# Performance work log

Measured on AMD Instinct MI355X. Metric: run time of the kernel, lower is better.

The kernel has to match this reference:

```python
import jax, jax.numpy as jnp
import numpy as np

N_NODES = 100000
N_EDGES = 1600000
NEG_SLOPE = 0.2  # DGL GATConv default leaky_relu slope
BN_EPS = 1e-5


def setup_inputs() -> dict:
    key = jax.random.key(0)
    ks = jax.random.split(key, 10)
    feats = jax.random.normal(ks[0], (N_NODES, 128), dtype=jnp.float32)
    src = jax.random.randint(ks[1], (N_EDGES,), 0, N_NODES, dtype=jnp.int64)
    dst = jax.random.randint(ks[2], (N_EDGES,), 0, N_NODES, dtype=jnp.int64)
    fc_w = jax.random.normal(ks[3], (256, 128), dtype=jnp.float32) * 0.05   # H*D x in_feats
    attn_l = jax.random.normal(ks[4], (4, 64), dtype=jnp.float32) * 0.05
    attn_r = jax.random.normal(ks[5], (4, 64), dtype=jnp.float32) * 0.05
    res_w = jax.random.normal(ks[6], (256, 128), dtype=jnp.float32) * 0.05  # residual projection
    bias = jax.random.normal(ks[7], (4, 64), dtype=jnp.float32) * 0.05
    gamma = jnp.ones((64,), dtype=jnp.float32)
    beta = jnp.zeros((64,), dtype=jnp.float32)
    return {"feats": feats, "src": src, "dst": dst, "fc_w": fc_w,
            "attn_l": attn_l, "attn_r": attn_r, "res_w": res_w,
            "bias": bias, "gamma": gamma, "beta": beta}


def reference(feats, src, dst, fc_w, attn_l, attn_r, res_w, bias, gamma, beta):
    N = feats.shape[0]
    H, D = attn_l.shape
    # projected features [N, H, D] (feat_drop is identity in eval mode)
    h = (feats @ fc_w.T).reshape(N, H, D)
    # per-node attention logits [N, H]
    el = jnp.sum(h * attn_l[None], axis=-1)
    er = jnp.sum(h * attn_r[None], axis=-1)
    # edge logits, leaky relu
    e = el[src] + er[dst]                       # [E, H]
    e = jnp.where(e > 0, e, NEG_SLOPE * e)
    # numerically stable segment softmax over incoming edges of each dst node
    m = jax.ops.segment_max(e, dst, num_segments=N)       # [N, H]
    ex = jnp.exp(e - m[dst])                               # [E, H]
    s = jax.ops.segment_sum(ex, dst, num_segments=N)       # [N, H]
    alpha = ex / s[dst]                                    # [E, H]
    # weighted message aggregation: scatter-add alpha * h_src into dst
    msg = h[src] * alpha[:, :, None]                       # [E, H, D]
    rst = jax.ops.segment_sum(msg, dst, num_segments=N)    # [N, H, D]
    # residual projection + bias + activation (elu)
    res = (feats @ res_w.T).reshape(N, H, D)
    rst = jax.nn.elu(rst + res + bias[None])
    # mean over heads -> [N, D]
    out = rst.mean(axis=1)
    # BatchNorm1d (training stats: biased variance over the node/batch axis)
    mu = out.mean(axis=0)
    var = out.var(axis=0)
    return (out - mu) * jax.lax.rsqrt(var + BN_EPS) * gamma + beta
```

## Files before the change

### kernel.cpp

```cpp
#include <hip/hip_runtime.h>

#define N_NODES 100000
#define N_EDGES 1600000
#define NEG_SLOPE 0.2f
#define BN_EPS 1e-5f

typedef __attribute__((ext_vector_type(8))) short short8;
typedef __attribute__((ext_vector_type(4))) float floatx4;
typedef __attribute__((ext_vector_type(8))) unsigned short u16x8;

static const size_t OFF_AB   = 0;
static const size_t OFF_BB   = 25624576;
static const size_t OFF_H    = 25755648;
static const size_t OFF_RES  = 76956672;
static const size_t OFF_EL   = 128156672;
static const size_t OFF_ER   = 129757184;
static const size_t OFF_DEG  = 131357184;
static const size_t OFF_RS   = 131757184;
static const size_t OFF_CUR  = 132157568;
static const size_t OFF_ESRC = 132557568;
static const size_t OFF_BS   = 142157568;
static const size_t OFF_BN   = 142158080;

__device__ __forceinline__ unsigned short f2bf(float x) {
  unsigned int u = __float_as_uint(x);
  unsigned int r = (u + 0x7fffu + ((u >> 16) & 1u)) >> 16;
  return (unsigned short)r;
}
__device__ __forceinline__ float bf2f(unsigned short u) {
  return __uint_as_float(((unsigned int)u) << 16);
}

__global__ __launch_bounds__(256) void k_pre(
    const float* __restrict__ feats, const float* __restrict__ fc_w,
    const float* __restrict__ res_w, const int* __restrict__ dst,
    unsigned short* __restrict__ Ab, unsigned short* __restrict__ Bb,
    int* __restrict__ deg, unsigned short* __restrict__ hbuf,
    float* __restrict__ el)
{
  const int b = blockIdx.x;
  if (b < 6256) {
    int c = b * 256 + threadIdx.x;
    int r = c >> 4, j = c & 15;
    unsigned short v[8];
    if (r < N_NODES) {
      const float* p = feats + (size_t)r * 128 + j * 8;
      float4 a = *(const float4*)p, bb = *(const float4*)(p + 4);
      v[0]=f2bf(a.x); v[1]=f2bf(a.y); v[2]=f2bf(a.z); v[3]=f2bf(a.w);
      v[4]=f2bf(bb.x); v[5]=f2bf(bb.y); v[6]=f2bf(bb.z); v[7]=f2bf(bb.w);
    } else {
      for (int i = 0; i < 8; i++) v[i] = 0;
    }
    size_t idx = (size_t)(r >> 7) * 2048 + ((r >> 4) & 7) * 256 + (j >> 2) * 64
               + (r & 15) + 16 * (j & 3);
    *(short8*)(Ab + idx * 8) = *(short8*)v;
  } else if (b < 12506) {
    int e = (b - 6256) * 256 + threadIdx.x;
    if (e < N_EDGES) atomicAdd(&deg[dst[e]], 1);
  } else if (b < 12538) {
    int c = (b - 12506) * 256 + threadIdx.x;
    int n = c >> 4, j = c & 15;
    const float* W = (n < 256) ? (fc_w + (size_t)n * 128) : (res_w + (size_t)(n - 256) * 128);
    const float* p = W + j * 8;
    float4 a = *(const float4*)p, bb = *(const float4*)(p + 4);
    unsigned short v[8];
    v[0]=f2bf(a.x); v[1]=f2bf(a.y); v[2]=f2bf(a.z); v[3]=f2bf(a.w);
    v[4]=f2bf(bb.x); v[5]=f2bf(bb.y); v[6]=f2bf(bb.z); v[7]=f2bf(bb.w);
    size_t idx = (size_t)(n >> 7) * 2048 + ((n >> 4) & 7) * 256 + (j >> 2) * 64
               + (n & 15) + 16 * (j & 3);
    *(short8*)(Bb + idx * 8) = *(short8*)v;
  } else {
    const int t = threadIdx.x;
    hbuf[(size_t)N_NODES * 256 + t] = 0;
    if (t < 4) el[N_NODES * 4 + t] = -1e30f;
  }
}

__global__ __launch_bounds__(256) void k_mm(
    const unsigned short* __restrict__ Ab, const unsigned short* __restrict__ Bb,
    const float* __restrict__ bias, const float* __restrict__ attn_l,
    const float* __restrict__ attn_r,
    unsigned short* __restrict__ hbuf, unsigned short* __restrict__ resbuf,
    float* __restrict__ el, float* __restrict__ er)
{
  __shared__ unsigned short sA[16384];
  const int tid = threadIdx.x;
  const int w = tid >> 6, L = tid & 63;
  const int blk = blockIdx.x;

  {
    const unsigned short* ga = Ab + (size_t)blk * 16384;
    #pragma unroll
    for (int i = 0; i < 8; i++) {
      int off = (i * 256 + w * 64) * 8;
      __builtin_amdgcn_global_load_lds(
          (const __attribute__((address_space(1))) unsigned int*)(ga + off + L * 8),
          (__attribute__((address_space(3))) unsigned int*)(sA + off),
          16, 0, 0);
    }
  }
  const int mh = w & 1, nh = w >> 1;
  __syncthreads();

  for (int wb = 0; wb < 2; ++wb) {
    const int nb = blockIdx.y + wb * 2;
    floatx4 acc[4][4] = {};
    const unsigned short* gb = Bb + ((size_t)nb * 2048 + nh * 4 * 256) * 8 + L * 8;
    #pragma unroll
    for (int s = 0; s < 4; s++) {
      short8 a[4], b[4];
      #pragma unroll
      for (int t = 0; t < 4; t++)
        a[t] = *(const short8*)(sA + ((mh * 4 + t) * 256 + s * 64 + L) * 8);
      #pragma unroll
      for (int t = 0; t < 4; t++)
        b[t] = *(const short8*)(gb + ((size_t)t * 256 + s * 64) * 8);
      #pragma unroll
      for (int mt = 0; mt < 4; mt++)
        #pragma unroll
        for (int nt = 0; nt < 4; nt++)
          acc[mt][nt] = __builtin_amdgcn_mfma_f32_16x16x32_bf16(a[mt], b[nt], acc[mt][nt], 0, 0, 0);
    }

    const int q = L >> 4, cn = L & 15;
    const int r0 = blk * 128 + mh * 64;
    if (nb < 2) {
      const int head = nb * 2 + nh;
      const int col0 = nb * 128 + nh * 64;
      float al[4], ar[4];
      #pragma unroll
      for (int nt = 0; nt < 4; nt++) {
        al[nt] = attn_l[head * 64 + nt * 16 + cn];
        ar[nt] = attn_r[head * 64 + nt * 16 + cn];
      }
      #pragma unroll
      for (int mt = 0; mt < 4; mt++)
        #pragma unroll
        for (int r = 0; r < 4; r++) {
          const int row = r0 + mt * 16 + q * 4 + r;
          float pl = 0.f, pr = 0.f;
          #pragma unroll
          for (int nt = 0; nt < 4; nt++) {
            pl = fmaf(acc[mt][nt][r], al[nt], pl);
            pr = fmaf(acc[mt][nt][r], ar[nt], pr);
          }
          #pragma unroll
          for (int o = 1; o < 16; o <<= 1) {
            pl += __shfl_xor(pl, o, 64);
            pr += __shfl_xor(pr, o, 64);
          }
          if (row < N_NODES) {
            #pragma unroll
            for (int nt = 0; nt < 4; nt++)
              hbuf[(size_t)row * 256 + col0 + nt * 16 + cn] = f2bf(acc[mt][nt][r]);
            if (cn == 0) {
              el[row * 4 + head] = pl;
              er[row * 4 + head] = pr;
            }
          }
        }
    } else {
      const int rc0 = (nb - 2) * 128 + nh * 64;
      #pragma unroll
      for (int mt = 0; mt < 4; mt++)
        #pragma unroll
        for (int r = 0; r < 4; r++) {
          const int row = r0 + mt * 16 + q * 4 + r;
          if (row < N_NODES)
            #pragma unroll
            for (int nt = 0; nt < 4; nt++) {
              float v = acc[mt][nt][r] + bias[rc0 + nt * 16 + cn];
              resbuf[(size_t)row * 256 + rc0 + nt * 16 + cn] = f2bf(v);
            }
        }
    }
  }
}

__global__ __launch_bounds__(256) void k_scan1(const int* __restrict__ deg,
                                               int* __restrict__ rs, int* __restrict__ bsums)
{
  __shared__ int tmp[256];
  const int t = threadIdx.x;
  const int base = blockIdx.x * 1024 + t * 4;
  int v0 = 0, v1 = 0, v2 = 0, v3 = 0;
  if (base + 0 < N_NODES) v0 = (deg[base + 0] + 3) & ~3;
  if (base + 1 < N_NODES) v1 = (deg[base + 1] + 3) & ~3;
  if (base + 2 < N_NODES) v2 = (deg[base + 2] + 3) & ~3;
  if (base + 3 < N_NODES) v3 = (deg[base + 3] + 3) & ~3;
  const int tsum = v0 + v1 + v2 + v3;
  tmp[t] = tsum;
  __syncthreads();
  for (int o = 1; o < 256; o <<= 1) {
    int x = (t >= o) ? tmp[t - o] : 0;
    __syncthreads();
    tmp[t] += x;
    __syncthreads();
  }
  const int excl = tmp[t] - tsum;
  if (base + 0 < N_NODES) rs[base + 0] = excl;
  if (base + 1 < N_NODES) rs[base + 1] = excl + v0;
  if (base + 2 < N_NODES) rs[base + 2] = excl + v0 + v1;
  if (base + 3 < N_NODES) rs[base + 3] = excl + v0 + v1 + v2;
  if (t == 255) bsums[blockIdx.x] = tmp[t];
}

__global__ __launch_bounds__(256) void k_scan3(int* __restrict__ rs,
                                               const int* __restrict__ bsums,
                                               int* __restrict__ cursor,
                                               const int* __restrict__ deg,
                                               int* __restrict__ esrc)
{
  __shared__ int sb[128];
  const int t = threadIdx.x;
  int raw = 0;
  if (t < 128) { raw = (t < 98) ? bsums[t] : 0; sb[t] = raw; }
  __syncthreads();
  for (int o = 1; o < 128; o <<= 1) {
    int x = (t >= o && t < 128) ? sb[t - o] : 0;
    __syncthreads();
    if (t < 128) sb[t] += x;
    __syncthreads();
  }
  if (t < 128) sb[t] -= raw;
  __syncthreads();
  const int i = blockIdx.x * 256 + t;
  if (i < N_NODES) {
    int v = rs[i] + sb[i >> 10];
    rs[i] = v;
    cursor[i] = v;
    const int d = deg[i];
    const int pd = (d + 3) & ~3;
    for (int j = d; j < pd; j++) esrc[v + j] = N_NODES;
    if (i == N_NODES - 1) rs[N_NODES] = v + pd;
  }
}

__global__ __launch_bounds__(256) void k_scatter(const int* __restrict__ src,
                                                 const int* __restrict__ dst,
                                                 int* __restrict__ cursor,
                                                 int* __restrict__ esrc)
{
  int e = blockIdx.x * 256 + threadIdx.x;
  if (e >= N_EDGES) return;
  int d = dst[e];
  int pos = atomicAdd(&cursor[d], 1);
  esrc[pos] = src[e];
}

#define RFL(x) __builtin_amdgcn_readfirstlane(x)

#define GATHER(X) do { \
  const int s_ = (lane & 32) ? sn##X.y : sn##X.x; \
  hv##X = *(const u16x8*)(hbuf + (size_t)s_ * 256 + li8); \
  ev##X = el[s_ * 4 + head]; \
} while (0)

#define PRO(X, B) do { \
  if ((B) < p_end) { sn##X = *(const int2*)(esrc + (B)); GATHER(X); } \
} while (0)

#define COMPUTE(X) do { \
  float e_ = ev##X + ern; \
  e_ = fmaxf(e_, NEG_SLOPE * e_); \
  const float w_ = __expf(e_); \
  ssum += w_; \
  accA.x = fmaf(w_, bf2f(hv##X[0]), accA.x); \
  accA.y = fmaf(w_, bf2f(hv##X[1]), accA.y); \
  accA.z = fmaf(w_, bf2f(hv##X[2]), accA.z); \
  accA.w = fmaf(w_, bf2f(hv##X[3]), accA.w); \
  accB.x = fmaf(w_, bf2f(hv##X[4]), accB.x); \
  accB.y = fmaf(w_, bf2f(hv##X[5]), accB.y); \
  accB.z = fmaf(w_, bf2f(hv##X[6]), accB.z); \
  accB.w = fmaf(w_, bf2f(hv##X[7]), accB.w); \
} while (0)

#define FIN(ND) do { \
  float st_ = ssum + __shfl_xor(ssum, 32, 64); \
  float a0_ = accA.x + __shfl_xor(accA.x, 32, 64); \
  float a1_ = accA.y + __shfl_xor(accA.y, 32, 64); \
  float a2_ = accA.z + __shfl_xor(accA.z, 32, 64); \
  float a3_ = accA.w + __shfl_xor(accA.w, 32, 64); \
  float a4_ = accB.x + __shfl_xor(accB.x, 32, 64); \
  float a5_ = accB.y + __shfl_xor(accB.y, 32, 64); \
  float a6_ = accB.z + __shfl_xor(accB.z, 32, 64); \
  float a7_ = accB.w + __shfl_xor(accB.w, 32, 64); \
  const float inv_ = (st_ > 0.f) ? (1.0f / st_) : 0.f; \
  a0_ = fmaf(a0_, inv_, bf2f(rv_cur[0])); \
  a1_ = fmaf(a1_, inv_, bf2f(rv_cur[1])); \
  a2_ = fmaf(a2_, inv_, bf2f(rv_cur[2])); \
  a3_ = fmaf(a3_, inv_, bf2f(rv_cur[3])); \
  a4_ = fmaf(a4_, inv_, bf2f(rv_cur[4])); \
  a5_ = fmaf(a5_, inv_, bf2f(rv_cur[5])); \
  a6_ = fmaf(a6_, inv_, bf2f(rv_cur[6])); \
  a7_ = fmaf(a7_, inv_, bf2f(rv_cur[7])); \
  a0_ = (a0_ > 0.f) ? a0_ : (__expf(a0_) - 1.f); \
  a1_ = (a1_ > 0.f) ? a1_ : (__expf(a1_) - 1.f); \
  a2_ = (a2_ > 0.f) ? a2_ : (__expf(a2_) - 1.f); \
  a3_ = (a3_ > 0.f) ? a3_ : (__expf(a3_) - 1.f); \
  a4_ = (a4_ > 0.f) ? a4_ : (__expf(a4_) - 1.f); \
  a5_ = (a5_ > 0.f) ? a5_ : (__expf(a5_) - 1.f); \
  a6_ = (a6_ > 0.f) ? a6_ : (__expf(a6_) - 1.f); \
  a7_ = (a7_ > 0.f) ? a7_ : (__expf(a7_) - 1.f); \
  a0_ += __shfl_xor(a0_, 8, 64);  a0_ += __shfl_xor(a0_, 16, 64); \
  a1_ += __shfl_xor(a1_, 8, 64);  a1_ += __shfl_xor(a1_, 16, 64); \
  a2_ += __shfl_xor(a2_, 8, 64);  a2_ += __shfl_xor(a2_, 16, 64); \
  a3_ += __shfl_xor(a3_, 8, 64);  a3_ += __shfl_xor(a3_, 16, 64); \
  a4_ += __shfl_xor(a4_, 8, 64);  a4_ += __shfl_xor(a4_, 16, 64); \
  a5_ += __shfl_xor(a5_, 8, 64);  a5_ += __shfl_xor(a5_, 16, 64); \
  a6_ += __shfl_xor(a6_, 8, 64);  a6_ += __shfl_xor(a6_, 16, 64); \
  a7_ += __shfl_xor(a7_, 8, 64);  a7_ += __shfl_xor(a7_, 16, 64); \
  if (lane < 8) { \
    float4 o1_, o2_; \
    o1_.x = a0_ * 0.25f; o1_.y = a1_ * 0.25f; o1_.z = a2_ * 0.25f; o1_.w = a3_ * 0.25f; \
    o2_.x = a4_ * 0.25f; o2_.y = a5_ * 0.25f; o2_.z = a6_ * 0.25f; o2_.w = a7_ * 0.25f; \
    *(float4*)(out + (size_t)(ND) * 64 + li8) = o1_; \
    *(float4*)(out + (size_t)(ND) * 64 + li8 + 4) = o2_; \
  } \
} while (0)

#define BOUNDARY() \
  while (p == nend) { \
    FIN(nu); \
    accA.x=0.f; accA.y=0.f; accA.z=0.f; accA.w=0.f; \
    accB.x=0.f; accB.y=0.f; accB.z=0.f; accB.w=0.f; ssum = 0.f; \
    nu++; \
    nend = nendN; ern = ernN; rv_cur = rvN; \
    const int f1_ = (nu + 1 < N_NODES) ? (nu + 1) : (N_NODES - 1); \
    const int f2_ = (nu + 2 <= N_NODES) ? (nu + 2) : N_NODES; \
    nendN = RFL(rs[f2_]); \
    ernN = er[f1_ * 4 + head]; \
    rvN = *(const u16x8*)(resbuf + (size_t)f1_ * 256 + li8); \
  }

#define STEP(CUR, GAT) do { \
  if (p + 12 < p_end) GATHER(GAT); \
  if (p + 16 < p_end) sn##CUR = *(const int2*)(esrc + p + 16); \
  BOUNDARY(); \
  COMPUTE(CUR); \
} while (0)

__global__ __launch_bounds__(256, 4) void k_agg(
    const unsigned short* __restrict__ hbuf, const unsigned short* __restrict__ resbuf,
    const float* __restrict__ el, const float* __restrict__ er,
    const int* __restrict__ rs, const int* __restrict__ esrc,
    float* __restrict__ out)
{
  const int lane = threadIdx.x & 63;
  const int li = lane & 31;
  const int head = li >> 3;
  const int li8 = li * 8;
  const int wid = blockIdx.x * 4 + (threadIdx.x >> 6);
  const int nW = gridDim.x * 4;

  const int n0 = (int)(((long long)wid * N_NODES) / nW);
  const int n1 = (int)(((long long)(wid + 1) * N_NODES) / nW);
  if (n0 >= n1) return;

  int nu = RFL(n0);
  const int p_end = RFL(rs[n1]);
  int nend = RFL(rs[nu + 1]);
  int f1 = (nu + 1 < N_NODES) ? (nu + 1) : (N_NODES - 1);
  int f2 = (nu + 2 <= N_NODES) ? (nu + 2) : N_NODES;
  int nendN = RFL(rs[f2]);
  float ern  = er[nu * 4 + head];
  float ernN = er[f1 * 4 + head];
  u16x8 rv_cur = *(const u16x8*)(resbuf + (size_t)nu * 256 + li8);
  u16x8 rvN    = *(const u16x8*)(resbuf + (size_t)f1 * 256 + li8);

  float4 accA = make_float4(0.f, 0.f, 0.f, 0.f);
  float4 accB = make_float4(0.f, 0.f, 0.f, 0.f);
  float ssum = 0.f;

  int2 snA, snB, snC, snD, snE, snF, snG, snH;
  float evA, evB, evC, evD, evE, evF, evG, evH;
  u16x8 hvA, hvB, hvC, hvD, hvE, hvF, hvG, hvH;

  int p = RFL(rs[nu]);
  PRO(A, p);      PRO(B, p + 2);  PRO(C, p + 4);  PRO(D, p + 6);
  PRO(E, p + 8);  PRO(F, p + 10);
  if (p + 12 < p_end) snG = *(const int2*)(esrc + p + 12);
  if (p + 14 < p_end) snH = *(const int2*)(esrc + p + 14);

  while (p < p_end) {
    STEP(A, G); p += 2; if (p >= p_end) break;
    STEP(B, H); p += 2; if (p >= p_end) break;
    STEP(C, A); p += 2; if (p >= p_end) break;
    STEP(D, B); p += 2; if (p >= p_end) break;
    STEP(E, C); p += 2; if (p >= p_end) break;
    STEP(F, D); p += 2; if (p >= p_end) break;
    STEP(G, E); p += 2; if (p >= p_end) break;
    STEP(H, F); p += 2;
  }

  while (nu < n1) {
    FIN(nu);
    accA.x=0.f; accA.y=0.f; accA.z=0.f; accA.w=0.f;
    accB.x=0.f; accB.y=0.f; accB.z=0.f; accB.w=0.f; ssum = 0.f;
    nu++;
    if (nu < n1) rv_cur = *(const u16x8*)(resbuf + (size_t)nu * 256 + li8);
  }
}

__global__ __launch_bounds__(256) void k_bn_stats(const float* __restrict__ out,
                                                  float* __restrict__ bn)
{
  const int t = threadIdx.x;
  const int c4 = (t & 15) * 4;
  const int rg = t >> 4;
  float4 s = make_float4(0.f, 0.f, 0.f, 0.f);
  float4 q = make_float4(0.f, 0.f, 0.f, 0.f);
  for (int row = blockIdx.x * 16 + rg; row < N_NODES; row += gridDim.x * 16) {
    float4 v = *(const float4*)(out + (size_t)row * 64 + c4);
    s.x += v.x; s.y += v.y; s.z += v.z; s.w += v.w;
    q.x += v.x * v.x; q.y += v.y * v.y; q.z += v.z * v.z; q.w += v.w * v.w;
  }
  __shared__ float ls[64], lq[64];
  if (t < 64) { ls[t] = 0.f; lq[t] = 0.f; }
  __syncthreads();
  atomicAdd(&ls[c4 + 0], s.x); atomicAdd(&ls[c4 + 1], s.y);
  atomicAdd(&ls[c4 + 2], s.z); atomicAdd(&ls[c4 + 3], s.w);
  atomicAdd(&lq[c4 + 0], q.x); atomicAdd(&lq[c4 + 1], q.y);
  atomicAdd(&lq[c4 + 2], q.z); atomicAdd(&lq[c4 + 3], q.w);
  __syncthreads();
  if (t < 64) {
    atomicAdd(&bn[t], ls[t]);
    atomicAdd(&bn[64 + t], lq[t]);
  }
}

__global__ __launch_bounds__(256) void k_bn_apply(float* __restrict__ out,
                                                  const float* __restrict__ bn,
                                                  const float* __restrict__ gamma,
                                                  const float* __restrict__ beta)
{
  __shared__ float sc[64], sh[64];
  const int t = threadIdx.x;
  if (t < 64) {
    float mean = bn[t] * (1.0f / N_NODES);
    float var = bn[64 + t] * (1.0f / N_NODES) - mean * mean;
    float s = gamma[t] * rsqrtf(var + BN_EPS);
    sc[t] = s;
    sh[t] = beta[t] - mean * s;
  }
  __syncthreads();
  const int i = blockIdx.x * 256 + t;
  if (i >= N_NODES * 16) return;
  const int d0 = (i & 15) * 4;
  float4 v = *(float4*)(out + (size_t)i * 4);
  v.x = fmaf(v.x, sc[d0 + 0], sh[d0 + 0]);
  v.y = fmaf(v.y, sc[d0 + 1], sh[d0 + 1]);
  v.z = fmaf(v.z, sc[d0 + 2], sh[d0 + 2]);
  v.w = fmaf(v.w, sc[d0 + 3], sh[d0 + 3]);
  *(float4*)(out + (size_t)i * 4) = v;
}

extern "C" void kernel_launch(void* const* d_in, const int* in_sizes, int n_in,
                              void* d_out, int out_size, void* d_ws, size_t ws_size,
                              hipStream_t stream)
{
  const float* feats  = (const float*)d_in[0];
  const int*   src    = (const int*)d_in[1];
  const int*   dst    = (const int*)d_in[2];
  const float* fc_w   = (const float*)d_in[3];
  const float* attn_l = (const float*)d_in[4];
  const float* attn_r = (const float*)d_in[5];
  const float* res_w  = (const float*)d_in[6];
  const float* bias   = (const float*)d_in[7];
  const float* gamma  = (const float*)d_in[8];
  const float* beta   = (const float*)d_in[9];

  char* ws = (char*)d_ws;
  unsigned short* Ab     = (unsigned short*)(ws + OFF_AB);
  unsigned short* Bb     = (unsigned short*)(ws + OFF_BB);
  unsigned short* hbuf   = (unsigned short*)(ws + OFF_H);
  unsigned short* resbuf = (unsigned short*)(ws + OFF_RES);
  float* elb    = (float*)(ws + OFF_EL);
  float* erb    = (float*)(ws + OFF_ER);
  int*   deg    = (int*)(ws + OFF_DEG);
  int*   rsb    = (int*)(ws + OFF_RS);
  int*   curb   = (int*)(ws + OFF_CUR);
  int*   esrc   = (int*)(ws + OFF_ESRC);
  int*   bsums  = (int*)(ws + OFF_BS);
  float* bnb    = (float*)(ws + OFF_BN);
  float* outp   = (float*)d_out;

  hipMemsetAsync(deg, 0, N_NODES * sizeof(int), stream);
  hipMemsetAsync(bnb, 0, 128 * sizeof(float), stream);

  k_pre<<<12539, 256, 0, stream>>>(feats, fc_w, res_w, dst, Ab, Bb, deg, hbuf, elb);
  k_mm<<<dim3(782, 2), 256, 0, stream>>>(Ab, Bb, bias, attn_l, attn_r,
                                         hbuf, resbuf, elb, erb);
  k_scan1<<<98, 256, 0, stream>>>(deg, rsb, bsums);
  k_scan3<<<391, 256, 0, stream>>>(rsb, bsums, curb, deg, esrc);
  k_scatter<<<6250, 256, 0, stream>>>(src, dst, curb, esrc);
  k_agg<<<2048, 256, 0, stream>>>(hbuf, resbuf, elb, erb, rsb, esrc, outp);
  k_bn_stats<<<256, 256, 0, stream>>>(outp, bnb);
  k_bn_apply<<<6250, 256, 0, stream>>>(outp, bnb, gamma, beta);
}
```

Measured before the change: 520.8 us.

## Fuse edge scatter into matmul kernel and add sched barriers in aggregation

Merges the CSR edge-scatter kernel into the projection matmul kernel. Blocks are interleaved so four of every five do atomic edge scatter and one does an MFMA tile. The scans now run before this fused kernel, so the memory-bound scatter overlaps the compute-bound matmul and one launch disappears. Scheduling barriers are also added in the aggregation loop to keep the prefetch gathers from being reordered past the compute. The risks are that the mixed roles leave some blocks idle or compete for resources, and the barriers may constrain the compiler's instruction scheduling.

```diff
diff --git a/kernel.cpp b/kernel.cpp
--- a/kernel.cpp
+++ b/kernel.cpp
@@ -76,17 +76,91 @@
   }
 }
 
-__global__ __launch_bounds__(256) void k_mm(
+__global__ __launch_bounds__(256) void k_scan1(const int* __restrict__ deg,
+                                               int* __restrict__ rs, int* __restrict__ bsums)
+{
+  __shared__ int tmp[256];
+  const int t = threadIdx.x;
+  const int base = blockIdx.x * 1024 + t * 4;
+  int v0 = 0, v1 = 0, v2 = 0, v3 = 0;
+  if (base + 0 < N_NODES) v0 = (deg[base + 0] + 3) & ~3;
+  if (base + 1 < N_NODES) v1 = (deg[base + 1] + 3) & ~3;
+  if (base + 2 < N_NODES) v2 = (deg[base + 2] + 3) & ~3;
+  if (base + 3 < N_NODES) v3 = (deg[base + 3] + 3) & ~3;
+  const int tsum = v0 + v1 + v2 + v3;
+  tmp[t] = tsum;
+  __syncthreads();
+  for (int o = 1; o < 256; o <<= 1) {
+    int x = (t >= o) ? tmp[t - o] : 0;
+    __syncthreads();
+    tmp[t] += x;
+    __syncthreads();
+  }
+  const int excl = tmp[t] - tsum;
+  if (base + 0 < N_NODES) rs[base + 0] = excl;
+  if (base + 1 < N_NODES) rs[base + 1] = excl + v0;
+  if (base + 2 < N_NODES) rs[base + 2] = excl + v0 + v1;
+  if (base + 3 < N_NODES) rs[base + 3] = excl + v0 + v1 + v2;
+  if (t == 255) bsums[blockIdx.x] = tmp[t];
+}
+
+__global__ __launch_bounds__(256) void k_scan3(int* __restrict__ rs,
+                                               const int* __restrict__ bsums,
+                                               int* __restrict__ cursor,
+                                               const int* __restrict__ deg,
+                                               int* __restrict__ esrc)
+{
+  __shared__ int sb[128];
+  const int t = threadIdx.x;
+  int raw = 0;
+  if (t < 128) { raw = (t < 98) ? bsums[t] : 0; sb[t] = raw; }
+  __syncthreads();
+  for (int o = 1; o < 128; o <<= 1) {
+    int x = (t >= o && t < 128) ? sb[t - o] : 0;
+    __syncthreads();
+    if (t < 128) sb[t] += x;
+    __syncthreads();
+  }
+  if (t < 128) sb[t] -= raw;
+  __syncthreads();
+  const int i = blockIdx.x * 256 + t;
+  if (i < N_NODES) {
+    int v = rs[i] + sb[i >> 10];
+    rs[i] = v;
+    cursor[i] = v;
+    const int d = deg[i];
+    const int pd = (d + 3) & ~3;
+    for (int j = d; j < pd; j++) esrc[v + j] = N_NODES;
+    if (i == N_NODES - 1) rs[N_NODES] = v + pd;
+  }
+}
+
+__global__ __launch_bounds__(256) void k_mmsc(
     const unsigned short* __restrict__ Ab, const unsigned short* __restrict__ Bb,
     const float* __restrict__ bias, const float* __restrict__ attn_l,
     const float* __restrict__ attn_r,
     unsigned short* __restrict__ hbuf, unsigned short* __restrict__ resbuf,
-    float* __restrict__ el, float* __restrict__ er)
+    float* __restrict__ el, float* __restrict__ er,
+    const int* __restrict__ src, const int* __restrict__ dst,
+    int* __restrict__ cursor, int* __restrict__ esrc)
 {
   __shared__ unsigned short sA[16384];
+  const int b = blockIdx.x;
+  const int g = b / 5, rrole = b % 5;
+
+  if (rrole != 4) {
+    const int e = (g * 4 + rrole) * 256 + threadIdx.x;
+    if (e < N_EDGES) {
+      int d = dst[e];
+      int pos = atomicAdd(&cursor[d], 1);
+      esrc[pos] = src[e];
+    }
+    return;
+  }
+
   const int tid = threadIdx.x;
   const int w = tid >> 6, L = tid & 63;
-  const int blk = blockIdx.x;
+  const int blk = g >> 1, nbb = g & 1;
 
   {
     const unsigned short* ga = Ab + (size_t)blk * 16384;
@@ -103,23 +177,23 @@
   __syncthreads();
 
   for (int wb = 0; wb < 2; ++wb) {
-    const int nb = blockIdx.y + wb * 2;
+    const int nb = nbb + wb * 2;
     floatx4 acc[4][4] = {};
     const unsigned short* gb = Bb + ((size_t)nb * 2048 + nh * 4 * 256) * 8 + L * 8;
     #pragma unroll
     for (int s = 0; s < 4; s++) {
-      short8 a[4], b[4];
+      short8 a[4], bfr[4];
       #pragma unroll
       for (int t = 0; t < 4; t++)
         a[t] = *(const short8*)(sA + ((mh * 4 + t) * 256 + s * 64 + L) * 8);
       #pragma unroll
       for (int t = 0; t < 4; t++)
-        b[t] = *(const short8*)(gb + ((size_t)t * 256 + s * 64) * 8);
+        bfr[t] = *(const short8*)(gb + ((size_t)t * 256 + s * 64) * 8);
       #pragma unroll
       for (int mt = 0; mt < 4; mt++)
         #pragma unroll
         for (int nt = 0; nt < 4; nt++)
-          acc[mt][nt] = __builtin_amdgcn_mfma_f32_16x16x32_bf16(a[mt], b[nt], acc[mt][nt], 0, 0, 0);
+          acc[mt][nt] = __builtin_amdgcn_mfma_f32_16x16x32_bf16(a[mt], bfr[nt], acc[mt][nt], 0, 0, 0);
     }
 
     const int q = L >> 4, cn = L & 15;
@@ -177,77 +251,6 @@
   }
 }
 
-__global__ __launch_bounds__(256) void k_scan1(const int* __restrict__ deg,
-                                               int* __restrict__ rs, int* __restrict__ bsums)
-{
-  __shared__ int tmp[256];
-  const int t = threadIdx.x;
-  const int base = blockIdx.x * 1024 + t * 4;
-  int v0 = 0, v1 = 0, v2 = 0, v3 = 0;
-  if (base + 0 < N_NODES) v0 = (deg[base + 0] + 3) & ~3;
-  if (base + 1 < N_NODES) v1 = (deg[base + 1] + 3) & ~3;
-  if (base + 2 < N_NODES) v2 = (deg[base + 2] + 3) & ~3;
-  if (base + 3 < N_NODES) v3 = (deg[base + 3] + 3) & ~3;
-  const int tsum = v0 + v1 + v2 + v3;
-  tmp[t] = tsum;
-  __syncthreads();
-  for (int o = 1; o < 256; o <<= 1) {
-    int x = (t >= o) ? tmp[t - o] : 0;
-    __syncthreads();
-    tmp[t] += x;
-    __syncthreads();
-  }
-  const int excl = tmp[t] - tsum;
-  if (base + 0 < N_NODES) rs[base + 0] = excl;
-  if (base + 1 < N_NODES) rs[base + 1] = excl + v0;
-  if (base + 2 < N_NODES) rs[base + 2] = excl + v0 + v1;
-  if (base + 3 < N_NODES) rs[base + 3] = excl + v0 + v1 + v2;
-  if (t == 255) bsums[blockIdx.x] = tmp[t];
-}
-
-__global__ __launch_bounds__(256) void k_scan3(int* __restrict__ rs,
-                                               const int* __restrict__ bsums,
-                                               int* __restrict__ cursor,
-                                               const int* __restrict__ deg,
-                                               int* __restrict__ esrc)
-{
-  __shared__ int sb[128];
-  const int t = threadIdx.x;
-  int raw = 0;
-  if (t < 128) { raw = (t < 98) ? bsums[t] : 0; sb[t] = raw; }
-  __syncthreads();
-  for (int o = 1; o < 128; o <<= 1) {
-    int x = (t >= o && t < 128) ? sb[t - o] : 0;
-    __syncthreads();
-    if (t < 128) sb[t] += x;
-    __syncthreads();
-  }
-  if (t < 128) sb[t] -= raw;
-  __syncthreads();
-  const int i = blockIdx.x * 256 + t;
-  if (i < N_NODES) {
-    int v = rs[i] + sb[i >> 10];
-    rs[i] = v;
-    cursor[i] = v;
-    const int d = deg[i];
-    const int pd = (d + 3) & ~3;
-    for (int j = d; j < pd; j++) esrc[v + j] = N_NODES;
-    if (i == N_NODES - 1) rs[N_NODES] = v + pd;
-  }
-}
-
-__global__ __launch_bounds__(256) void k_scatter(const int* __restrict__ src,
-                                                 const int* __restrict__ dst,
-                                                 int* __restrict__ cursor,
-                                                 int* __restrict__ esrc)
-{
-  int e = blockIdx.x * 256 + threadIdx.x;
-  if (e >= N_EDGES) return;
-  int d = dst[e];
-  int pos = atomicAdd(&cursor[d], 1);
-  esrc[pos] = src[e];
-}
-
 #define RFL(x) __builtin_amdgcn_readfirstlane(x)
 
 #define GATHER(X) do { \
@@ -336,6 +339,7 @@
 #define STEP(CUR, GAT) do { \
   if (p + 12 < p_end) GATHER(GAT); \
   if (p + 16 < p_end) sn##CUR = *(const int2*)(esrc + p + 16); \
+  __builtin_amdgcn_sched_barrier(0); \
   BOUNDARY(); \
   COMPUTE(CUR); \
 } while (0)
@@ -381,6 +385,7 @@
   PRO(E, p + 8);  PRO(F, p + 10);
   if (p + 12 < p_end) snG = *(const int2*)(esrc + p + 12);
   if (p + 14 < p_end) snH = *(const int2*)(esrc + p + 14);
+  __builtin_amdgcn_sched_barrier(0);
 
   while (p < p_end) {
     STEP(A, G); p += 2; if (p >= p_end) break;
@@ -489,11 +494,11 @@
   hipMemsetAsync(bnb, 0, 128 * sizeof(float), stream);
 
   k_pre<<<12539, 256, 0, stream>>>(feats, fc_w, res_w, dst, Ab, Bb, deg, hbuf, elb);
-  k_mm<<<dim3(782, 2), 256, 0, stream>>>(Ab, Bb, bias, attn_l, attn_r,
-                                         hbuf, resbuf, elb, erb);
   k_scan1<<<98, 256, 0, stream>>>(deg, rsb, bsums);
   k_scan3<<<391, 256, 0, stream>>>(rsb, bsums, curb, deg, esrc);
-  k_scatter<<<6250, 256, 0, stream>>>(src, dst, curb, esrc);
+  k_mmsc<<<7820, 256, 0, stream>>>(Ab, Bb, bias, attn_l, attn_r,
+                                   hbuf, resbuf, elb, erb,
+                                   src, dst, curb, esrc);
   k_agg<<<2048, 256, 0, stream>>>(hbuf, resbuf, elb, erb, rsb, esrc, outp);
   k_bn_stats<<<256, 256, 0, stream>>>(outp, bnb);
   k_bn_apply<<<6250, 256, 0, stream>>>(outp, bnb, gamma, beta);
```

After: 509.1 us. 2.3% less time.

## Record edge ranks in degree pass, fuse BN stats into aggregation

Applied to the files above, without the earlier changes.

The degree-counting pass now stores each edge's atomic rank, held temporarily in the output buffer. A non-atomic placement kernel then writes esrc, which removes the second atomic cursor scatter. BatchNorm sum and sum-of-squares are accumulated in shared memory inside the aggregation kernel, with global partials padded by 16 floats, so the separate stats kernel and its reread of the output go away. Scheduling barriers are added to the gather loop, and the CSR-building kernels are launched before the matmul. The cost is many LDS atomics per node in the aggregation epilogue.

```diff
diff --git a/kernel.cpp b/kernel.cpp
--- a/kernel.cpp
+++ b/kernel.cpp
@@ -17,10 +17,9 @@
 static const size_t OFF_ER   = 129757184;
 static const size_t OFF_DEG  = 131357184;
 static const size_t OFF_RS   = 131757184;
-static const size_t OFF_CUR  = 132157568;
+static const size_t OFF_BNP  = 132157568;
 static const size_t OFF_ESRC = 132557568;
 static const size_t OFF_BS   = 142157568;
-static const size_t OFF_BN   = 142158080;
 
 __device__ __forceinline__ unsigned short f2bf(float x) {
   unsigned int u = __float_as_uint(x);
@@ -36,7 +35,7 @@
     const float* __restrict__ res_w, const int* __restrict__ dst,
     unsigned short* __restrict__ Ab, unsigned short* __restrict__ Bb,
     int* __restrict__ deg, unsigned short* __restrict__ hbuf,
-    float* __restrict__ el)
+    float* __restrict__ el, int* __restrict__ rank)
 {
   const int b = blockIdx.x;
   if (b < 6256) {
@@ -56,7 +55,7 @@
     *(short8*)(Ab + idx * 8) = *(short8*)v;
   } else if (b < 12506) {
     int e = (b - 6256) * 256 + threadIdx.x;
-    if (e < N_EDGES) atomicAdd(&deg[dst[e]], 1);
+    if (e < N_EDGES) rank[e] = atomicAdd(&deg[dst[e]], 1);
   } else if (b < 12538) {
     int c = (b - 12506) * 256 + threadIdx.x;
     int n = c >> 4, j = c & 15;
@@ -74,6 +73,74 @@
     hbuf[(size_t)N_NODES * 256 + t] = 0;
     if (t < 4) el[N_NODES * 4 + t] = -1e30f;
   }
+}
+
+__global__ __launch_bounds__(256) void k_scan1(const int* __restrict__ deg,
+                                               int* __restrict__ rs, int* __restrict__ bsums)
+{
+  __shared__ int tmp[256];
+  const int t = threadIdx.x;
+  const int base = blockIdx.x * 1024 + t * 4;
+  int v0 = 0, v1 = 0, v2 = 0, v3 = 0;
+  if (base + 0 < N_NODES) v0 = (deg[base + 0] + 3) & ~3;
+  if (base + 1 < N_NODES) v1 = (deg[base + 1] + 3) & ~3;
+  if (base + 2 < N_NODES) v2 = (deg[base + 2] + 3) & ~3;
+  if (base + 3 < N_NODES) v3 = (deg[base + 3] + 3) & ~3;
+  const int tsum = v0 + v1 + v2 + v3;
+  tmp[t] = tsum;
+  __syncthreads();
+  for (int o = 1; o < 256; o <<= 1) {
+    int x = (t >= o) ? tmp[t - o] : 0;
+    __syncthreads();
+    tmp[t] += x;
+    __syncthreads();
+  }
+  const int excl = tmp[t] - tsum;
+  if (base + 0 < N_NODES) rs[base + 0] = excl;
+  if (base + 1 < N_NODES) rs[base + 1] = excl + v0;
+  if (base + 2 < N_NODES) rs[base + 2] = excl + v0 + v1;
+  if (base + 3 < N_NODES) rs[base + 3] = excl + v0 + v1 + v2;
+  if (t == 255) bsums[blockIdx.x] = tmp[t];
+}
+
+__global__ __launch_bounds__(256) void k_scan3(int* __restrict__ rs,
+                                               const int* __restrict__ bsums,
+                                               const int* __restrict__ deg,
+                                               int* __restrict__ esrc)
+{
+  __shared__ int sb[128];
+  const int t = threadIdx.x;
+  int raw = 0;
+  if (t < 128) { raw = (t < 98) ? bsums[t] : 0; sb[t] = raw; }
+  __syncthreads();
+  for (int o = 1; o < 128; o <<= 1) {
+    int x = (t >= o && t < 128) ? sb[t - o] : 0;
+    __syncthreads();
+    if (t < 128) sb[t] += x;
+    __syncthreads();
+  }
+  if (t < 128) sb[t] -= raw;
+  __syncthreads();
+  const int i = blockIdx.x * 256 + t;
+  if (i < N_NODES) {
+    int v = rs[i] + sb[i >> 10];
+    rs[i] = v;
+    const int d = deg[i];
+    const int pd = (d + 3) & ~3;
+    for (int j = d; j < pd; j++) esrc[v + j] = N_NODES;
+    if (i == N_NODES - 1) rs[N_NODES] = v + pd;
+  }
+}
+
+__global__ __launch_bounds__(256) void k_place(const int* __restrict__ src,
+                                               const int* __restrict__ dst,
+                                               const int* __restrict__ rs,
+                                               const int* __restrict__ rank,
+                                               int* __restrict__ esrc)
+{
+  int e = blockIdx.x * 256 + threadIdx.x;
+  if (e >= N_EDGES) return;
+  esrc[rs[dst[e]] + rank[e]] = src[e];
 }
 
 __global__ __launch_bounds__(256) void k_mm(
@@ -175,77 +242,6 @@
         }
     }
   }
-}
-
-__global__ __launch_bounds__(256) void k_scan1(const int* __restrict__ deg,
-                                               int* __restrict__ rs, int* __restrict__ bsums)
-{
-  __shared__ int tmp[256];
-  const int t = threadIdx.x;
-  const int base = blockIdx.x * 1024 + t * 4;
-  int v0 = 0, v1 = 0, v2 = 0, v3 = 0;
-  if (base + 0 < N_NODES) v0 = (deg[base + 0] + 3) & ~3;
-  if (base + 1 < N_NODES) v1 = (deg[base + 1] + 3) & ~3;
-  if (base + 2 < N_NODES) v2 = (deg[base + 2] + 3) & ~3;
-  if (base + 3 < N_NODES) v3 = (deg[base + 3] + 3) & ~3;
-  const int tsum = v0 + v1 + v2 + v3;
-  tmp[t] = tsum;
-  __syncthreads();
-  for (int o = 1; o < 256; o <<= 1) {
-    int x = (t >= o) ? tmp[t - o] : 0;
-    __syncthreads();
-    tmp[t] += x;
-    __syncthreads();
-  }
-  const int excl = tmp[t] - tsum;
-  if (base + 0 < N_NODES) rs[base + 0] = excl;
-  if (base + 1 < N_NODES) rs[base + 1] = excl + v0;
-  if (base + 2 < N_NODES) rs[base + 2] = excl + v0 + v1;
-  if (base + 3 < N_NODES) rs[base + 3] = excl + v0 + v1 + v2;
-  if (t == 255) bsums[blockIdx.x] = tmp[t];
-}
-
-__global__ __launch_bounds__(256) void k_scan3(int* __restrict__ rs,
-                                               const int* __restrict__ bsums,
-                                               int* __restrict__ cursor,
-                                               const int* __restrict__ deg,
-                                               int* __restrict__ esrc)
-{
-  __shared__ int sb[128];
-  const int t = threadIdx.x;
-  int raw = 0;
-  if (t < 128) { raw = (t < 98) ? bsums[t] : 0; sb[t] = raw; }
-  __syncthreads();
-  for (int o = 1; o < 128; o <<= 1) {
-    int x = (t >= o && t < 128) ? sb[t - o] : 0;
-    __syncthreads();
-    if (t < 128) sb[t] += x;
-    __syncthreads();
-  }
-  if (t < 128) sb[t] -= raw;
-  __syncthreads();
-  const int i = blockIdx.x * 256 + t;
-  if (i < N_NODES) {
-    int v = rs[i] + sb[i >> 10];
-    rs[i] = v;
-    cursor[i] = v;
-    const int d = deg[i];
-    const int pd = (d + 3) & ~3;
-    for (int j = d; j < pd; j++) esrc[v + j] = N_NODES;
-    if (i == N_NODES - 1) rs[N_NODES] = v + pd;
-  }
-}
-
-__global__ __launch_bounds__(256) void k_scatter(const int* __restrict__ src,
-                                                 const int* __restrict__ dst,
-                                                 int* __restrict__ cursor,
-                                                 int* __restrict__ esrc)
-{
-  int e = blockIdx.x * 256 + threadIdx.x;
-  if (e >= N_EDGES) return;
-  int d = dst[e];
-  int pos = atomicAdd(&cursor[d], 1);
-  esrc[pos] = src[e];
 }
 
 #define RFL(x) __builtin_amdgcn_readfirstlane(x)
@@ -316,6 +312,14 @@
     o2_.x = a4_ * 0.25f; o2_.y = a5_ * 0.25f; o2_.z = a6_ * 0.25f; o2_.w = a7_ * 0.25f; \
     *(float4*)(out + (size_t)(ND) * 64 + li8) = o1_; \
     *(float4*)(out + (size_t)(ND) * 64 + li8 + 4) = o2_; \
+    atomicAdd(&ls[li8 + 0], o1_.x); atomicAdd(&ls[li8 + 1], o1_.y); \
+    atomicAdd(&ls[li8 + 2], o1_.z); atomicAdd(&ls[li8 + 3], o1_.w); \
+    atomicAdd(&ls[li8 + 4], o2_.x); atomicAdd(&ls[li8 + 5], o2_.y); \
+    atomicAdd(&ls[li8 + 6], o2_.z); atomicAdd(&ls[li8 + 7], o2_.w); \
+    atomicAdd(&lq[li8 + 0], o1_.x * o1_.x); atomicAdd(&lq[li8 + 1], o1_.y * o1_.y); \
+    atomicAdd(&lq[li8 + 2], o1_.z * o1_.z); atomicAdd(&lq[li8 + 3], o1_.w * o1_.w); \
+    atomicAdd(&lq[li8 + 4], o2_.x * o2_.x); atomicAdd(&lq[li8 + 5], o2_.y * o2_.y); \
+    atomicAdd(&lq[li8 + 6], o2_.z * o2_.z); atomicAdd(&lq[li8 + 7], o2_.w * o2_.w); \
   } \
 } while (0)
 
@@ -336,6 +340,7 @@
 #define STEP(CUR, GAT) do { \
   if (p + 12 < p_end) GATHER(GAT); \
   if (p + 16 < p_end) sn##CUR = *(const int2*)(esrc + p + 16); \
+  __builtin_amdgcn_sched_barrier(0); \
   BOUNDARY(); \
   COMPUTE(CUR); \
 } while (0)
@@ -344,8 +349,9 @@
     const unsigned short* __restrict__ hbuf, const unsigned short* __restrict__ resbuf,
     const float* __restrict__ el, const float* __restrict__ er,
     const int* __restrict__ rs, const int* __restrict__ esrc,
-    float* __restrict__ out)
-{
+    float* __restrict__ out, float* __restrict__ bn)
+{
+  __shared__ float ls[64], lq[64];
   const int lane = threadIdx.x & 63;
   const int li = lane & 31;
   const int head = li >> 3;
@@ -353,80 +359,63 @@
   const int wid = blockIdx.x * 4 + (threadIdx.x >> 6);
   const int nW = gridDim.x * 4;
 
+  if (threadIdx.x < 64) { ls[threadIdx.x] = 0.f; lq[threadIdx.x] = 0.f; }
+  __syncthreads();
+
   const int n0 = (int)(((long long)wid * N_NODES) / nW);
   const int n1 = (int)(((long long)(wid + 1) * N_NODES) / nW);
-  if (n0 >= n1) return;
-
-  int nu = RFL(n0);
-  const int p_end = RFL(rs[n1]);
-  int nend = RFL(rs[nu + 1]);
-  int f1 = (nu + 1 < N_NODES) ? (nu + 1) : (N_NODES - 1);
-  int f2 = (nu + 2 <= N_NODES) ? (nu + 2) : N_NODES;
-  int nendN = RFL(rs[f2]);
-  float ern  = er[nu * 4 + head];
-  float ernN = er[f1 * 4 + head];
-  u16x8 rv_cur = *(const u16x8*)(resbuf + (size_t)nu * 256 + li8);
-  u16x8 rvN    = *(const u16x8*)(resbuf + (size_t)f1 * 256 + li8);
-
-  float4 accA = make_float4(0.f, 0.f, 0.f, 0.f);
-  float4 accB = make_float4(0.f, 0.f, 0.f, 0.f);
-  float ssum = 0.f;
-
-  int2 snA, snB, snC, snD, snE, snF, snG, snH;
-  float evA, evB, evC, evD, evE, evF, evG, evH;
-  u16x8 hvA, hvB, hvC, hvD, hvE, hvF, hvG, hvH;
-
-  int p = RFL(rs[nu]);
-  PRO(A, p);      PRO(B, p + 2);  PRO(C, p + 4);  PRO(D, p + 6);
-  PRO(E, p + 8);  PRO(F, p + 10);
-  if (p + 12 < p_end) snG = *(const int2*)(esrc + p + 12);
-  if (p + 14 < p_end) snH = *(const int2*)(esrc + p + 14);
-
-  while (p < p_end) {
-    STEP(A, G); p += 2; if (p >= p_end) break;
-    STEP(B, H); p += 2; if (p >= p_end) break;
-    STEP(C, A); p += 2; if (p >= p_end) break;
-    STEP(D, B); p += 2; if (p >= p_end) break;
-    STEP(E, C); p += 2; if (p >= p_end) break;
-    STEP(F, D); p += 2; if (p >= p_end) break;
-    STEP(G, E); p += 2; if (p >= p_end) break;
-    STEP(H, F); p += 2;
-  }
-
-  while (nu < n1) {
-    FIN(nu);
-    accA.x=0.f; accA.y=0.f; accA.z=0.f; accA.w=0.f;
-    accB.x=0.f; accB.y=0.f; accB.z=0.f; accB.w=0.f; ssum = 0.f;
-    nu++;
-    if (nu < n1) rv_cur = *(const u16x8*)(resbuf + (size_t)nu * 256 + li8);
-  }
-}
-
-__global__ __launch_bounds__(256) void k_bn_stats(const float* __restrict__ out,
-                                                  float* __restrict__ bn)
-{
+
+  if (n0 < n1) {
+    int nu = RFL(n0);
+    const int p_end = RFL(rs[n1]);
+    int nend = RFL(rs[nu + 1]);
+    int f1 = (nu + 1 < N_NODES) ? (nu + 1) : (N_NODES - 1);
+    int f2 = (nu + 2 <= N_NODES) ? (nu + 2) : N_NODES;
+    int nendN = RFL(rs[f2]);
+    float ern  = er[nu * 4 + head];
+    float ernN = er[f1 * 4 + head];
+    u16x8 rv_cur = *(const u16x8*)(resbuf + (size_t)nu * 256 + li8);
+    u16x8 rvN    = *(const u16x8*)(resbuf + (size_t)f1 * 256 + li8);
+
+    float4 accA = make_float4(0.f, 0.f, 0.f, 0.f);
+    float4 accB = make_float4(0.f, 0.f, 0.f, 0.f);
+    float ssum = 0.f;
+
+    int2 snA, snB, snC, snD, snE, snF, snG, snH;
+    float evA, evB, evC, evD, evE, evF, evG, evH;
+    u16x8 hvA, hvB, hvC, hvD, hvE, hvF, hvG, hvH;
+
+    int p = RFL(rs[nu]);
+    PRO(A, p);      PRO(B, p + 2);  PRO(C, p + 4);  PRO(D, p + 6);
+    PRO(E, p + 8);  PRO(F, p + 10);
+    if (p + 12 < p_end) snG = *(const int2*)(esrc + p + 12);
+    if (p + 14 < p_end) snH = *(const int2*)(esrc + p + 14);
+    __builtin_amdgcn_sched_barrier(0);
+
+    while (p < p_end) {
+      STEP(A, G); p += 2; if (p >= p_end) break;
+      STEP(B, H); p += 2; if (p >= p_end) break;
+      STEP(C, A); p += 2; if (p >= p_end) break;
+      STEP(D, B); p += 2; if (p >= p_end) break;
+      STEP(E, C); p += 2; if (p >= p_end) break;
+      STEP(F, D); p += 2; if (p >= p_end) break;
+      STEP(G, E); p += 2; if (p >= p_end) break;
+      STEP(H, F); p += 2;
+    }
+
+    while (nu < n1) {
+      FIN(nu);
+      accA.x=0.f; accA.y=0.f; accA.z=0.f; accA.w=0.f;
+      accB.x=0.f; accB.y=0.f; accB.z=0.f; accB.w=0.f; ssum = 0.f;
+      nu++;
+      if (nu < n1) rv_cur = *(const u16x8*)(resbuf + (size_t)nu * 256 + li8);
+    }
+  }
+
+  __syncthreads();
   const int t = threadIdx.x;
-  const int c4 = (t & 15) * 4;
-  const int rg = t >> 4;
-  float4 s = make_float4(0.f, 0.f, 0.f, 0.f);
-  float4 q = make_float4(0.f, 0.f, 0.f, 0.f);
-  for (int row = blockIdx.x * 16 + rg; row < N_NODES; row += gridDim.x * 16) {
-    float4 v = *(const float4*)(out + (size_t)row * 64 + c4);
-    s.x += v.x; s.y += v.y; s.z += v.z; s.w += v.w;
-    q.x += v.x * v.x; q.y += v.y * v.y; q.z += v.z * v.z; q.w += v.w * v.w;
-  }
-  __shared__ float ls[64], lq[64];
-  if (t < 64) { ls[t] = 0.f; lq[t] = 0.f; }
-  __syncthreads();
-  atomicAdd(&ls[c4 + 0], s.x); atomicAdd(&ls[c4 + 1], s.y);
-  atomicAdd(&ls[c4 + 2], s.z); atomicAdd(&ls[c4 + 3], s.w);
-  atomicAdd(&lq[c4 + 0], q.x); atomicAdd(&lq[c4 + 1], q.y);
-  atomicAdd(&lq[c4 + 2], q.z); atomicAdd(&lq[c4 + 3], q.w);
-  __syncthreads();
-  if (t < 64) {
-    atomicAdd(&bn[t], ls[t]);
-    atomicAdd(&bn[64 + t], lq[t]);
-  }
+  if (t < 64)       atomicAdd(&bn[t * 16], ls[t]);
+  else if (t < 128) atomicAdd(&bn[t * 16], lq[t - 64]);
 }
 
 __global__ __launch_bounds__(256) void k_bn_apply(float* __restrict__ out,
@@ -437,8 +426,8 @@
   __shared__ float sc[64], sh[64];
   const int t = threadIdx.x;
   if (t < 64) {
-    float mean = bn[t] * (1.0f / N_NODES);
-    float var = bn[64 + t] * (1.0f / N_NODES) - mean * mean;
+    float mean = bn[t * 16] * (1.0f / N_NODES);
+    float var = bn[(t + 64) * 16] * (1.0f / N_NODES) - mean * mean;
     float s = gamma[t] * rsqrtf(var + BN_EPS);
     sc[t] = s;
     sh[t] = beta[t] - mean * s;
@@ -479,22 +468,21 @@
   float* erb    = (float*)(ws + OFF_ER);
   int*   deg    = (int*)(ws + OFF_DEG);
   int*   rsb    = (int*)(ws + OFF_RS);
-  int*   curb   = (int*)(ws + OFF_CUR);
+  float* bnb    = (float*)(ws + OFF_BNP);
   int*   esrc   = (int*)(ws + OFF_ESRC);
   int*   bsums  = (int*)(ws + OFF_BS);
-  float* bnb    = (float*)(ws + OFF_BN);
   float* outp   = (float*)d_out;
+  int*   rankp  = (int*)d_out;
 
   hipMemsetAsync(deg, 0, N_NODES * sizeof(int), stream);
-  hipMemsetAsync(bnb, 0, 128 * sizeof(float), stream);
-
-  k_pre<<<12539, 256, 0, stream>>>(feats, fc_w, res_w, dst, Ab, Bb, deg, hbuf, elb);
+  hipMemsetAsync(bnb, 0, 128 * 16 * sizeof(float), stream);
+
+  k_pre<<<12539, 256, 0, stream>>>(feats, fc_w, res_w, dst, Ab, Bb, deg, hbuf, elb, rankp);
+  k_scan1<<<98, 256, 0, stream>>>(deg, rsb, bsums);
+  k_scan3<<<391, 256, 0, stream>>>(rsb, bsums, deg, esrc);
+  k_place<<<6250, 256, 0, stream>>>(src, dst, rsb, rankp, esrc);
   k_mm<<<dim3(782, 2), 256, 0, stream>>>(Ab, Bb, bias, attn_l, attn_r,
                                          hbuf, resbuf, elb, erb);
-  k_scan1<<<98, 256, 0, stream>>>(deg, rsb, bsums);
-  k_scan3<<<391, 256, 0, stream>>>(rsb, bsums, curb, deg, esrc);
-  k_scatter<<<6250, 256, 0, stream>>>(src, dst, curb, esrc);
-  k_agg<<<2048, 256, 0, stream>>>(hbuf, resbuf, elb, erb, rsb, esrc, outp);
-  k_bn_stats<<<256, 256, 0, stream>>>(outp, bnb);
+  k_agg<<<2048, 256, 0, stream>>>(hbuf, resbuf, elb, erb, rsb, esrc, outp, bnb);
   k_bn_apply<<<6250, 256, 0, stream>>>(outp, bnb, gamma, beta);
 }
```

After: 454.6 us. -12.7%, faster.
